# Kernel optimization log

Hardware: AMD Instinct MI355X
Metric: run time of the kernel (lower is better)

The kernel has to match this reference:

```python
import jax, jax.numpy as jnp
import numpy as np

N, D, E, K = 16384, 4096, 128, 2

def setup_inputs() -> dict:
    key = jax.random.key(0)
    k1, k2 = jax.random.split(key)
    x = jax.random.normal(k1, (N, D), dtype=jnp.float32)
    W = jax.random.normal(k2, (E, D), dtype=jnp.float32) * (1.0 / np.sqrt(D))
    b = jnp.zeros((E,), dtype=jnp.float32)
    return {"x": x, "W": W, "b": b}

def reference(x, W, b):
    # logits = x @ W.T + b  -> [N, E]
    logits = jnp.einsum('nd,ed->ne', x, W) + b
    confidence = jax.nn.sigmoid(logits)
    top_k_vals, top_k_indices = jax.lax.top_k(confidence, K)  # [N, K]
    return top_k_vals, top_k_indices
```

## Files before the change

kernel.cpp:

```cpp
#include <hip/hip_runtime.h>
#include <stdint.h>
#include <math.h>

#define N_ROWS 16384
#define D_DIM  4096
#define E_EXP  128
#define BM     32
#define BKR    128
#define NR     (D_DIM / BKR)
#define TAU    2.5e-4f

typedef short  short8 __attribute__((ext_vector_type(8)));
typedef float  f32x4  __attribute__((ext_vector_type(4)));

__device__ __forceinline__ uint32_t bf16_rne(float f) {
  uint32_t u = __builtin_bit_cast(uint32_t, f);
  return (u + 0x7fffu + ((u >> 16) & 1u)) >> 16;
}

__global__ __launch_bounds__(256) void k0_split(const float* __restrict__ W,
                                                uint16_t* __restrict__ wt) {
  const int b  = blockIdx.x;
  const int t  = threadIdx.x;
  const int eg  = b >> 5;
  const int kcg = b & 31;
  const int kc  = kcg * 4 + (t >> 6);
  const int lane = t & 63;
  const int e  = eg * 16 + (lane & 15);
  const int k0 = kc * 32 + (lane >> 4) * 8;

  const float* src = W + (size_t)e * D_DIM + k0;
  f32x4 w0 = *(const f32x4*)src;
  f32x4 w1 = *(const f32x4*)(src + 4);
  float wf[8] = {w0[0], w0[1], w0[2], w0[3], w1[0], w1[1], w1[2], w1[3]};

  uint16_t h[8], l[8];
  #pragma unroll
  for (int j = 0; j < 8; ++j) {
    uint32_t hh = bf16_rne(wf[j]);
    float hf = __builtin_bit_cast(float, hh << 16);
    h[j] = (uint16_t)hh;
    l[j] = (uint16_t)bf16_rne(wf[j] - hf);
  }
  const size_t blkh = ((size_t)(eg * 128 + kc) * 2 + 0) * 512;
  const size_t blkl = ((size_t)(eg * 128 + kc) * 2 + 1) * 512;
  *(short8*)(wt + blkh + lane * 8) = *(const short8*)h;
  *(short8*)(wt + blkl + lane * 8) = *(const short8*)l;
}

__global__ __launch_bounds__(512, 4) void k1_main(
    const float* __restrict__ x, const uint16_t* __restrict__ wt,
    const float* __restrict__ bias, float* __restrict__ out, int* __restrict__ flags)
{
  __shared__ __align__(16) uint8_t smem[32768];
  float* Ld = (float*)smem;

  const int t    = threadIdx.x;
  const int lane = t & 63;
  const int wv   = __builtin_amdgcn_readfirstlane(t >> 6);
  const int row0 = blockIdx.x * BM;

  const int srow = t >> 4;
  const int skg  = t & 15;
  const float* xp = x + (size_t)(row0 + srow) * D_DIM + skg * 8;

  const int s_w = skg >> 2, gg_w = skg & 3, rr_w = srow & 15, rg_w = srow >> 4;
  const int p_w  = gg_w * 16 + (rr_w ^ (gg_w << 1) ^ s_w);
  const int wa_h = (s_w * 4 + rg_w * 2 + 0) * 1024 + p_w * 16;
  const int wa_l = wa_h + 1024;

  const int ggr = lane >> 4, rrr = lane & 15;
  const int p_r0 = ggr * 16 + (rrr ^ (ggr << 1));

  const short8* Wt8 = (const short8*)wt;
  const int ccol = lane & 15;
  const size_t wbase0 = ((size_t)(wv * 128) * 2) * 64 + lane;

  f32x4 acc[2] = {};

  f32x4 xa0, xa1, xb0, xb1, xc0, xc1;
  xa0 = *((const f32x4*)xp + 0); xa1 = *((const f32x4*)xp + 1);
  xb0 = *((const f32x4*)(xp + BKR) + 0); xb1 = *((const f32x4*)(xp + BKR) + 1);

  short8 Wc[8], Wn[8];
  #pragma unroll
  for (int q = 0; q < 8; ++q) Wc[q] = Wt8[wbase0 + (size_t)q * 64];

  #pragma unroll 2
  for (int r = 0; r < NR; ++r) {
    if (r + 1 < NR) {
      const size_t nb = ((size_t)(wv * 128 + (r + 1) * 4) * 2) * 64 + lane;
      #pragma unroll
      for (int q = 0; q < 8; ++q) Wn[q] = Wt8[nb + (size_t)q * 64];
    }
    if (r + 2 < NR) {
      const f32x4* np = (const f32x4*)(xp + (size_t)(r + 2) * BKR);
      xc0 = np[0]; xc1 = np[1];
    }
    __builtin_amdgcn_sched_barrier(0);

    float xf[8] = {xa0[0], xa0[1], xa0[2], xa0[3], xa1[0], xa1[1], xa1[2], xa1[3]};
    uint32_t hpk[4], lpk[4];
    #pragma unroll
    for (int j = 0; j < 4; ++j) {
      uint32_t h0 = bf16_rne(xf[2*j]), h1 = bf16_rne(xf[2*j+1]);
      float h0f = __builtin_bit_cast(float, h0 << 16);
      float h1f = __builtin_bit_cast(float, h1 << 16);
      uint32_t l0 = bf16_rne(xf[2*j] - h0f), l1 = bf16_rne(xf[2*j+1] - h1f);
      hpk[j] = h0 | (h1 << 16);
      lpk[j] = l0 | (l1 << 16);
    }
    uint8_t* buf = smem + (r & 1) * 16384;
    *(uint4*)(buf + wa_h) = make_uint4(hpk[0], hpk[1], hpk[2], hpk[3]);
    *(uint4*)(buf + wa_l) = make_uint4(lpk[0], lpk[1], lpk[2], lpk[3]);

    xa0 = xb0; xa1 = xb1; xb0 = xc0; xb1 = xc1;

    asm volatile("s_waitcnt lgkmcnt(0)" ::: "memory");
    __builtin_amdgcn_s_barrier();

    __builtin_amdgcn_s_setprio(1);
    #pragma unroll
    for (int s = 0; s < 4; ++s) {
      const int pr = p_r0 ^ s;
      const short8 bh = Wc[s * 2 + 0], bl = Wc[s * 2 + 1];
      #pragma unroll
      for (int rg = 0; rg < 2; ++rg) {
        const uint8_t* fb = buf + (s * 4 + rg * 2) * 1024 + pr * 16;
        short8 ah = *(const short8*)fb;
        short8 al = *(const short8*)(fb + 1024);
        acc[rg] = __builtin_amdgcn_mfma_f32_16x16x32_bf16(ah, bh, acc[rg], 0, 0, 0);
        acc[rg] = __builtin_amdgcn_mfma_f32_16x16x32_bf16(al, bh, acc[rg], 0, 0, 0);
        acc[rg] = __builtin_amdgcn_mfma_f32_16x16x32_bf16(ah, bl, acc[rg], 0, 0, 0);
      }
    }
    __builtin_amdgcn_s_setprio(0);

    #pragma unroll
    for (int q = 0; q < 8; ++q) Wc[q] = Wn[q];
  }

  float b0 = bias[wv * 16 + ccol];
  __syncthreads();
  #pragma unroll
  for (int rg = 0; rg < 2; ++rg)
    #pragma unroll
    for (int i = 0; i < 4; ++i) {
      int row = rg * 16 + ggr * 4 + i;
      int e = wv * 16 + ccol;
      Ld[row * 128 + e] = acc[rg][i] + b0;
    }
  __syncthreads();

  {
    const int row = t >> 4, part = t & 15;
    float l1 = -3e38f, l2 = -3e38f, l3 = -3e38f;
    int   i1 = -1, i2 = -1, i3 = -1;
    auto ins = [&](float v, int e) {
      if (v > l1 || (v == l1 && e < i1)) { l3=l2; i3=i2; l2=l1; i2=i1; l1=v; i1=e; }
      else if (v > l2 || (v == l2 && e < i2)) { l3=l2; i3=i2; l2=v; i2=e; }
      else if (v > l3 || (v == l3 && e < i3)) { l3=v; i3=e; }
    };
    #pragma unroll
    for (int j = 0; j < 2; ++j) {
      const float* pp = Ld + row * 128 + part * 8 + j * 4;
      f32x4 v = *(const f32x4*)pp;
      int eb = part * 8 + j * 4;
      ins(v[0], eb); ins(v[1], eb + 1); ins(v[2], eb + 2); ins(v[3], eb + 3);
    }
    #pragma unroll
    for (int m = 1; m <= 8; m <<= 1) {
      float a1 = __shfl_xor(l1, m), a2 = __shfl_xor(l2, m), a3 = __shfl_xor(l3, m);
      int   b1i = __shfl_xor(i1, m), b2i = __shfl_xor(i2, m), b3i = __shfl_xor(i3, m);
      ins(a1, b1i); ins(a2, b2i); ins(a3, b3i);
    }
    if (part == 0) {
      int grow = row0 + row;
      int fl = ((l1 - l2) < TAU) || ((l2 - l3) < TAU);
      flags[grow] = fl;
      out[(size_t)grow * 2 + 0] = 1.f / (1.f + __expf(-l1));
      out[(size_t)grow * 2 + 1] = 1.f / (1.f + __expf(-l2));
      out[(size_t)N_ROWS * 2 + (size_t)grow * 2 + 0] = (float)i1;
      out[(size_t)N_ROWS * 2 + (size_t)grow * 2 + 1] = (float)i2;
    }
  }
}

__global__ __launch_bounds__(1024) void k2_fix(
    const float* __restrict__ x, const float* __restrict__ W,
    const float* __restrict__ bias, const int* __restrict__ flags,
    float* __restrict__ out)
{
  __shared__ double lgs[E_EXP];
  const int t    = threadIdx.x;
  const int wvi  = t >> 6, lane = t & 63;
  const int e    = wvi * 8 + (lane >> 3);
  const int sub  = lane & 7;
  const int rbase = blockIdx.x * 8;

  for (int rr = 0; rr < 8; ++rr) {
    const int row = rbase + rr;
    if (!flags[row]) continue;
    const float* xr = x + (size_t)row * D_DIM;
    const float* wr = W + (size_t)e * D_DIM;
    double a0 = 0.0, a1 = 0.0, a2 = 0.0, a3 = 0.0;
    for (int j = 0; j < 128; ++j) {
      const int c4 = (j * 8 + sub) * 4;
      f32x4 xv = *(const f32x4*)(xr + c4);
      f32x4 wvv = *(const f32x4*)(wr + c4);
      a0 += (double)xv[0] * wvv[0];
      a1 += (double)xv[1] * wvv[1];
      a2 += (double)xv[2] * wvv[2];
      a3 += (double)xv[3] * wvv[3];
    }
    double acc = (a0 + a1) + (a2 + a3);
    #pragma unroll
    for (int m = 1; m <= 4; m <<= 1) acc += __shfl_xor(acc, m);
    if (sub == 0) lgs[e] = acc + (double)bias[e];
    __syncthreads();
    if (t == 0) {
      double l1 = -1e300, l2 = -1e300; int i1 = -1, i2 = -1;
      for (int ee = 0; ee < E_EXP; ++ee) {
        double v = lgs[ee];
        if (v > l1) { l2 = l1; i2 = i1; l1 = v; i1 = ee; }
        else if (v > l2) { l2 = v; i2 = ee; }
      }
      out[(size_t)row * 2 + 0] = (float)(1.0 / (1.0 + exp(-l1)));
      out[(size_t)row * 2 + 1] = (float)(1.0 / (1.0 + exp(-l2)));
      out[(size_t)N_ROWS * 2 + (size_t)row * 2 + 0] = (float)i1;
      out[(size_t)N_ROWS * 2 + (size_t)row * 2 + 1] = (float)i2;
    }
    __syncthreads();
  }
}

extern "C" void kernel_launch(void* const* d_in, const int* in_sizes, int n_in,
                              void* d_out, int out_size, void* d_ws, size_t ws_size,
                              hipStream_t stream) {
  const float* x  = (const float*)d_in[0];
  const float* Wm = (const float*)d_in[1];
  const float* b  = (const float*)d_in[2];
  float* out = (float*)d_out;

  uint16_t* wt = (uint16_t*)d_ws;
  int* flags = (int*)((uint8_t*)d_ws + 2u * 1024 * 1024);

  k0_split<<<dim3(256), dim3(256), 0, stream>>>(Wm, wt);
  k1_main<<<dim3(N_ROWS / BM), dim3(512), 0, stream>>>(x, wt, b, out, flags);
  k2_fix<<<dim3(N_ROWS / 8), dim3(1024), 0, stream>>>(x, Wm, b, flags, out);
}
```

Measured before the change: 178.5 us.

## Stream x tiles into LDS via async global_load_lds with 4-stage ring

Replaces the register-staged prefetch of x (two tiles ahead held in VGPRs) with direct global-to-LDS async loads into a four-buffer ring, keeping three tiles in flight. Each iteration converts the raw fp32 tile from LDS into the bf16 hi/lo fragment buffer, then runs the MFMAs. The aim is deeper memory pipelining and lower VGPR pressure. In exchange, LDS per block grows from 32KB to 80KB, which limits blocks per CU, and each iteration adds an extra barrier and LDS round trip. The s_setprio hints are also removed.

```diff
diff --git a/kernel.cpp b/kernel.cpp
--- a/kernel.cpp
+++ b/kernel.cpp
@@ -12,6 +12,13 @@
 
 typedef short  short8 __attribute__((ext_vector_type(8)));
 typedef float  f32x4  __attribute__((ext_vector_type(4)));
+
+#define GAS __attribute__((address_space(1)))
+#define LAS __attribute__((address_space(3)))
+
+__device__ __forceinline__ void g2lds16(const float* g, uint8_t* l) {
+  __builtin_amdgcn_global_load_lds((const GAS uint32_t*)g, (LAS uint32_t*)l, 16, 0, 0);
+}
 
 __device__ __forceinline__ uint32_t bf16_rne(float f) {
   uint32_t u = __builtin_bit_cast(uint32_t, f);
@@ -52,19 +59,26 @@
     const float* __restrict__ x, const uint16_t* __restrict__ wt,
     const float* __restrict__ bias, float* __restrict__ out, int* __restrict__ flags)
 {
-  __shared__ __align__(16) uint8_t smem[32768];
+  __shared__ __align__(16) uint8_t smem[81920];
   float* Ld = (float*)smem;
+  uint8_t* fragb = smem + 65536;
 
   const int t    = threadIdx.x;
   const int lane = t & 63;
   const int wv   = __builtin_amdgcn_readfirstlane(t >> 6);
   const int row0 = blockIdx.x * BM;
 
-  const int srow = t >> 4;
-  const int skg  = t & 15;
-  const float* xp = x + (size_t)(row0 + srow) * D_DIM + skg * 8;
-
-  const int s_w = skg >> 2, gg_w = skg & 3, rr_w = srow & 15, rg_w = srow >> 4;
+  const int G1 = t, G2 = 512 + t;
+  const int sr1 = G1 >> 5, sg1 = (G1 & 31) ^ (sr1 & 7);
+  const int sr2 = G2 >> 5, sg2 = (G2 & 31) ^ (sr2 & 7);
+  const float* xsrc1 = x + (size_t)(row0 + sr1) * D_DIM + sg1 * 4;
+  const float* xsrc2 = x + (size_t)(row0 + sr2) * D_DIM + sg2 * 4;
+
+  const int lr = t >> 4, lg = t & 15;
+  const int rg0 = (lr * 32 + ((lg * 2 + 0) ^ (lr & 7))) * 16;
+  const int rg1 = (lr * 32 + ((lg * 2 + 1) ^ (lr & 7))) * 16;
+
+  const int s_w = lg >> 2, gg_w = lg & 3, rr_w = lr & 15, rg_w = lr >> 4;
   const int p_w  = gg_w * 16 + (rr_w ^ (gg_w << 1) ^ s_w);
   const int wa_h = (s_w * 4 + rg_w * 2 + 0) * 1024 + p_w * 16;
   const int wa_l = wa_h + 1024;
@@ -74,59 +88,71 @@
 
   const short8* Wt8 = (const short8*)wt;
   const int ccol = lane & 15;
-  const size_t wbase0 = ((size_t)(wv * 128) * 2) * 64 + lane;
 
   f32x4 acc[2] = {};
 
-  f32x4 xa0, xa1, xb0, xb1, xc0, xc1;
-  xa0 = *((const f32x4*)xp + 0); xa1 = *((const f32x4*)xp + 1);
-  xb0 = *((const f32x4*)(xp + BKR) + 0); xb1 = *((const f32x4*)(xp + BKR) + 1);
+  g2lds16(xsrc1 + 0 * BKR, smem + 0 * 16384 + G1 * 16);
+  g2lds16(xsrc2 + 0 * BKR, smem + 0 * 16384 + G2 * 16);
+  g2lds16(xsrc1 + 1 * BKR, smem + 1 * 16384 + G1 * 16);
+  g2lds16(xsrc2 + 1 * BKR, smem + 1 * 16384 + G2 * 16);
+  g2lds16(xsrc1 + 2 * BKR, smem + 2 * 16384 + G1 * 16);
+  g2lds16(xsrc2 + 2 * BKR, smem + 2 * 16384 + G2 * 16);
 
   short8 Wc[8], Wn[8];
-  #pragma unroll
-  for (int q = 0; q < 8; ++q) Wc[q] = Wt8[wbase0 + (size_t)q * 64];
+  {
+    const size_t base0 = ((size_t)(wv * 128) * 2) * 64 + lane;
+    #pragma unroll
+    for (int q = 0; q < 8; ++q) Wc[q] = Wt8[base0 + (size_t)q * 64];
+  }
 
   #pragma unroll 2
   for (int r = 0; r < NR; ++r) {
+    __builtin_amdgcn_s_barrier();
+
     if (r + 1 < NR) {
       const size_t nb = ((size_t)(wv * 128 + (r + 1) * 4) * 2) * 64 + lane;
       #pragma unroll
       for (int q = 0; q < 8; ++q) Wn[q] = Wt8[nb + (size_t)q * 64];
     }
-    if (r + 2 < NR) {
-      const f32x4* np = (const f32x4*)(xp + (size_t)(r + 2) * BKR);
-      xc0 = np[0]; xc1 = np[1];
-    }
+    if (r + 3 < NR) {
+      const int rr = r + 3;
+      uint8_t* rb = smem + (rr & 3) * 16384;
+      g2lds16(xsrc1 + (size_t)rr * BKR, rb + G1 * 16);
+      g2lds16(xsrc2 + (size_t)rr * BKR, rb + G2 * 16);
+    }
+    asm volatile("s_waitcnt vmcnt(12)" ::: "memory");
     __builtin_amdgcn_sched_barrier(0);
 
-    float xf[8] = {xa0[0], xa0[1], xa0[2], xa0[3], xa1[0], xa1[1], xa1[2], xa1[3]};
-    uint32_t hpk[4], lpk[4];
-    #pragma unroll
-    for (int j = 0; j < 4; ++j) {
-      uint32_t h0 = bf16_rne(xf[2*j]), h1 = bf16_rne(xf[2*j+1]);
-      float h0f = __builtin_bit_cast(float, h0 << 16);
-      float h1f = __builtin_bit_cast(float, h1 << 16);
-      uint32_t l0 = bf16_rne(xf[2*j] - h0f), l1 = bf16_rne(xf[2*j+1] - h1f);
-      hpk[j] = h0 | (h1 << 16);
-      lpk[j] = l0 | (l1 << 16);
-    }
-    uint8_t* buf = smem + (r & 1) * 16384;
-    *(uint4*)(buf + wa_h) = make_uint4(hpk[0], hpk[1], hpk[2], hpk[3]);
-    *(uint4*)(buf + wa_l) = make_uint4(lpk[0], lpk[1], lpk[2], lpk[3]);
-
-    xa0 = xb0; xa1 = xb1; xb0 = xc0; xb1 = xc1;
+    {
+      const uint8_t* rb = smem + (r & 3) * 16384;
+      f32x4 a = *(const f32x4*)(rb + rg0);
+      f32x4 b = *(const f32x4*)(rb + rg1);
+      float xf[8] = {a[0], a[1], a[2], a[3], b[0], b[1], b[2], b[3]};
+      uint32_t hpk[4], lpk[4];
+      #pragma unroll
+      for (int j = 0; j < 4; ++j) {
+        uint32_t h0 = bf16_rne(xf[2*j]), h1 = bf16_rne(xf[2*j+1]);
+        float h0f = __builtin_bit_cast(float, h0 << 16);
+        float h1f = __builtin_bit_cast(float, h1 << 16);
+        uint32_t l0 = bf16_rne(xf[2*j] - h0f), l1 = bf16_rne(xf[2*j+1] - h1f);
+        hpk[j] = h0 | (h1 << 16);
+        lpk[j] = l0 | (l1 << 16);
+      }
+      *(uint4*)(fragb + wa_h) = make_uint4(hpk[0], hpk[1], hpk[2], hpk[3]);
+      *(uint4*)(fragb + wa_l) = make_uint4(lpk[0], lpk[1], lpk[2], lpk[3]);
+    }
 
     asm volatile("s_waitcnt lgkmcnt(0)" ::: "memory");
     __builtin_amdgcn_s_barrier();
-
-    __builtin_amdgcn_s_setprio(1);
+    __builtin_amdgcn_sched_barrier(0);
+
     #pragma unroll
     for (int s = 0; s < 4; ++s) {
       const int pr = p_r0 ^ s;
       const short8 bh = Wc[s * 2 + 0], bl = Wc[s * 2 + 1];
       #pragma unroll
       for (int rg = 0; rg < 2; ++rg) {
-        const uint8_t* fb = buf + (s * 4 + rg * 2) * 1024 + pr * 16;
+        const uint8_t* fb = fragb + (s * 4 + rg * 2) * 1024 + pr * 16;
         short8 ah = *(const short8*)fb;
         short8 al = *(const short8*)(fb + 1024);
         acc[rg] = __builtin_amdgcn_mfma_f32_16x16x32_bf16(ah, bh, acc[rg], 0, 0, 0);
@@ -134,13 +160,13 @@
         acc[rg] = __builtin_amdgcn_mfma_f32_16x16x32_bf16(ah, bl, acc[rg], 0, 0, 0);
       }
     }
-    __builtin_amdgcn_s_setprio(0);
 
     #pragma unroll
     for (int q = 0; q < 8; ++q) Wc[q] = Wn[q];
   }
 
   float b0 = bias[wv * 16 + ccol];
+  asm volatile("s_waitcnt vmcnt(0)" ::: "memory");
   __syncthreads();
   #pragma unroll
   for (int rg = 0; rg < 2; ++rg)
```

Measured after the change: 184.5 us. 1.03x slower.

## Software-pipeline x staging so LDS writes for next tile overlap MFMA compute

Applied to the files above, without the earlier changes.

Restructures the main loop so the tile for step r+1 is converted to bf16 hi/lo and written to the other LDS buffer after the MFMAs for step r. The first tile is staged in a prologue. The x prefetch distance grows from two to three tiles ahead. The setprio/sched_barrier hints are removed. The aim is to hide the conversion, LDS-store and global-load latency behind MFMA work, at the cost of more live registers, which may reduce occupancy.

```diff
diff --git a/kernel.cpp b/kernel.cpp
--- a/kernel.cpp
+++ b/kernel.cpp
@@ -74,32 +74,12 @@
 
   const short8* Wt8 = (const short8*)wt;
   const int ccol = lane & 15;
-  const size_t wbase0 = ((size_t)(wv * 128) * 2) * 64 + lane;
 
   f32x4 acc[2] = {};
 
-  f32x4 xa0, xa1, xb0, xb1, xc0, xc1;
-  xa0 = *((const f32x4*)xp + 0); xa1 = *((const f32x4*)xp + 1);
-  xb0 = *((const f32x4*)(xp + BKR) + 0); xb1 = *((const f32x4*)(xp + BKR) + 1);
-
-  short8 Wc[8], Wn[8];
-  #pragma unroll
-  for (int q = 0; q < 8; ++q) Wc[q] = Wt8[wbase0 + (size_t)q * 64];
-
-  #pragma unroll 2
-  for (int r = 0; r < NR; ++r) {
-    if (r + 1 < NR) {
-      const size_t nb = ((size_t)(wv * 128 + (r + 1) * 4) * 2) * 64 + lane;
-      #pragma unroll
-      for (int q = 0; q < 8; ++q) Wn[q] = Wt8[nb + (size_t)q * 64];
-    }
-    if (r + 2 < NR) {
-      const f32x4* np = (const f32x4*)(xp + (size_t)(r + 2) * BKR);
-      xc0 = np[0]; xc1 = np[1];
-    }
-    __builtin_amdgcn_sched_barrier(0);
-
-    float xf[8] = {xa0[0], xa0[1], xa0[2], xa0[3], xa1[0], xa1[1], xa1[2], xa1[3]};
+  {
+    f32x4 t0 = *((const f32x4*)xp + 0), t1 = *((const f32x4*)xp + 1);
+    float xf[8] = {t0[0], t0[1], t0[2], t0[3], t1[0], t1[1], t1[2], t1[3]};
     uint32_t hpk[4], lpk[4];
     #pragma unroll
     for (int j = 0; j < 4; ++j) {
@@ -110,23 +90,55 @@
       hpk[j] = h0 | (h1 << 16);
       lpk[j] = l0 | (l1 << 16);
     }
-    uint8_t* buf = smem + (r & 1) * 16384;
-    *(uint4*)(buf + wa_h) = make_uint4(hpk[0], hpk[1], hpk[2], hpk[3]);
-    *(uint4*)(buf + wa_l) = make_uint4(lpk[0], lpk[1], lpk[2], lpk[3]);
-
-    xa0 = xb0; xa1 = xb1; xb0 = xc0; xb1 = xc1;
-
-    asm volatile("s_waitcnt lgkmcnt(0)" ::: "memory");
-    __builtin_amdgcn_s_barrier();
-
-    __builtin_amdgcn_s_setprio(1);
+    *(uint4*)(smem + wa_h) = make_uint4(hpk[0], hpk[1], hpk[2], hpk[3]);
+    *(uint4*)(smem + wa_l) = make_uint4(lpk[0], lpk[1], lpk[2], lpk[3]);
+  }
+  f32x4 xa0, xa1, xb0, xb1, xc0, xc1;
+  xa0 = *((const f32x4*)(xp + 1 * BKR) + 0); xa1 = *((const f32x4*)(xp + 1 * BKR) + 1);
+  xb0 = *((const f32x4*)(xp + 2 * BKR) + 0); xb1 = *((const f32x4*)(xp + 2 * BKR) + 1);
+  xc0 = *((const f32x4*)(xp + 3 * BKR) + 0); xc1 = *((const f32x4*)(xp + 3 * BKR) + 1);
+
+  short8 Wc[8], Wn[8];
+  {
+    const size_t b0 = ((size_t)(wv * 128) * 2) * 64 + lane;
+    #pragma unroll
+    for (int q = 0; q < 8; ++q) Wc[q] = Wt8[b0 + (size_t)q * 64];
+  }
+  asm volatile("s_waitcnt lgkmcnt(0)" ::: "memory");
+  __builtin_amdgcn_s_barrier();
+
+  #pragma unroll 2
+  for (int r = 0; r < NR; ++r) {
+    uint8_t* rbuf = smem + (r & 1) * 16384;
+    uint8_t* wbuf = smem + ((r + 1) & 1) * 16384;
+
+    if (r + 1 < NR) {
+      const size_t nb = ((size_t)(wv * 128 + (r + 1) * 4) * 2) * 64 + lane;
+      #pragma unroll
+      for (int q = 0; q < 8; ++q) Wn[q] = Wt8[nb + (size_t)q * 64];
+    }
+
+    uint32_t hpk[4], lpk[4];
+    if (r + 1 < NR) {
+      float xf[8] = {xa0[0], xa0[1], xa0[2], xa0[3], xa1[0], xa1[1], xa1[2], xa1[3]};
+      #pragma unroll
+      for (int j = 0; j < 4; ++j) {
+        uint32_t h0 = bf16_rne(xf[2*j]), h1 = bf16_rne(xf[2*j+1]);
+        float h0f = __builtin_bit_cast(float, h0 << 16);
+        float h1f = __builtin_bit_cast(float, h1 << 16);
+        uint32_t l0 = bf16_rne(xf[2*j] - h0f), l1 = bf16_rne(xf[2*j+1] - h1f);
+        hpk[j] = h0 | (h1 << 16);
+        lpk[j] = l0 | (l1 << 16);
+      }
+    }
+
     #pragma unroll
     for (int s = 0; s < 4; ++s) {
       const int pr = p_r0 ^ s;
       const short8 bh = Wc[s * 2 + 0], bl = Wc[s * 2 + 1];
       #pragma unroll
       for (int rg = 0; rg < 2; ++rg) {
-        const uint8_t* fb = buf + (s * 4 + rg * 2) * 1024 + pr * 16;
+        const uint8_t* fb = rbuf + (s * 4 + rg * 2) * 1024 + pr * 16;
         short8 ah = *(const short8*)fb;
         short8 al = *(const short8*)(fb + 1024);
         acc[rg] = __builtin_amdgcn_mfma_f32_16x16x32_bf16(ah, bh, acc[rg], 0, 0, 0);
@@ -134,7 +146,20 @@
         acc[rg] = __builtin_amdgcn_mfma_f32_16x16x32_bf16(ah, bl, acc[rg], 0, 0, 0);
       }
     }
-    __builtin_amdgcn_s_setprio(0);
+
+    if (r + 1 < NR) {
+      *(uint4*)(wbuf + wa_h) = make_uint4(hpk[0], hpk[1], hpk[2], hpk[3]);
+      *(uint4*)(wbuf + wa_l) = make_uint4(lpk[0], lpk[1], lpk[2], lpk[3]);
+    }
+
+    xa0 = xb0; xa1 = xb1; xb0 = xc0; xb1 = xc1;
+    if (r + 4 < NR) {
+      const f32x4* np = (const f32x4*)(xp + (size_t)(r + 4) * BKR);
+      xc0 = np[0]; xc1 = np[1];
+    }
+
+    asm volatile("s_waitcnt lgkmcnt(0)" ::: "memory");
+    __builtin_amdgcn_s_barrier();
 
     #pragma unroll
     for (int q = 0; q < 8; ++q) Wc[q] = Wn[q];
```

Result: faster. 170.8 us (-4.3%).

## Stage x tiles via async global-to-LDS loads with triple buffer and LDS counter sync

Applied to the files above, without the earlier changes.

The main kernel now handles 64 rows per block. Each wave computes a 32-row by 32-expert quadrant, so every W fragment it loads feeds two row groups. Raw fp32 x tiles are copied straight into a swizzled three-slot LDS ring with global_load_lds. Each wave does its own bf16 hi/lo split after reading from LDS, and W fragments are loaded per step instead of being double-buffered in registers. Block-wide barriers are replaced by spin-waits on LDS atomic counters (staged/done), aiming for better load/compute overlap. The trade-offs are more LDS per block (about 96KB) and therefore lower occupancy, redundant hi/lo conversion work, and spin-wait overhead.

```diff
diff --git a/kernel.cpp b/kernel.cpp
--- a/kernel.cpp
+++ b/kernel.cpp
@@ -5,13 +5,21 @@
 #define N_ROWS 16384
 #define D_DIM  4096
 #define E_EXP  128
-#define BM     32
+#define BM     64
 #define BKR    128
 #define NR     (D_DIM / BKR)
+#define NW     8
 #define TAU    2.5e-4f
 
 typedef short  short8 __attribute__((ext_vector_type(8)));
 typedef float  f32x4  __attribute__((ext_vector_type(4)));
+
+#define GAS __attribute__((address_space(1)))
+#define LAS __attribute__((address_space(3)))
+
+__device__ __forceinline__ void g2lds16(const float* g, uint8_t* l) {
+  __builtin_amdgcn_global_load_lds((const GAS uint32_t*)g, (LAS uint32_t*)l, 16, 0, 0);
+}
 
 __device__ __forceinline__ uint32_t bf16_rne(float f) {
   uint32_t u = __builtin_bit_cast(uint32_t, f);
@@ -48,112 +56,131 @@
   *(short8*)(wt + blkl + lane * 8) = *(const short8*)l;
 }
 
-__global__ __launch_bounds__(512, 4) void k1_main(
+__global__ __launch_bounds__(512) void k1_main(
     const float* __restrict__ x, const uint16_t* __restrict__ wt,
     const float* __restrict__ bias, float* __restrict__ out, int* __restrict__ flags)
 {
-  __shared__ __align__(16) uint8_t smem[32768];
+  __shared__ __align__(16) uint8_t smem[3 * 32768 + 256];
+  int* done   = (int*)(smem + 98304);
+  int* staged = done + 32;
   float* Ld = (float*)smem;
 
   const int t    = threadIdx.x;
   const int lane = t & 63;
   const int wv   = __builtin_amdgcn_readfirstlane(t >> 6);
+  const int rh   = wv >> 2;
+  const int eq   = wv & 3;
   const int row0 = blockIdx.x * BM;
-
-  const int srow = t >> 4;
-  const int skg  = t & 15;
-  const float* xp = x + (size_t)(row0 + srow) * D_DIM + skg * 8;
-
-  const int s_w = skg >> 2, gg_w = skg & 3, rr_w = srow & 15, rg_w = srow >> 4;
-  const int p_w  = gg_w * 16 + (rr_w ^ (gg_w << 1) ^ s_w);
-  const int wa_h = (s_w * 4 + rg_w * 2 + 0) * 1024 + p_w * 16;
-  const int wa_l = wa_h + 1024;
-
-  const int ggr = lane >> 4, rrr = lane & 15;
-  const int p_r0 = ggr * 16 + (rrr ^ (ggr << 1));
+  const int r15  = lane & 15, kg = lane >> 4;
 
   const short8* Wt8 = (const short8*)wt;
-  const int ccol = lane & 15;
-  const size_t wbase0 = ((size_t)(wv * 128) * 2) * 64 + lane;
-
-  f32x4 acc[2] = {};
-
-  f32x4 xa0, xa1, xb0, xb1, xc0, xc1;
-  xa0 = *((const f32x4*)xp + 0); xa1 = *((const f32x4*)xp + 1);
-  xb0 = *((const f32x4*)(xp + BKR) + 0); xb1 = *((const f32x4*)(xp + BKR) + 1);
-
-  short8 Wc[8], Wn[8];
-  #pragma unroll
-  for (int q = 0; q < 8; ++q) Wc[q] = Wt8[wbase0 + (size_t)q * 64];
-
-  #pragma unroll 2
+
+  auto stageTile = [&](int tile) {
+    uint8_t* base = smem + (tile % 3) * 32768;
+    #pragma unroll
+    for (int i = 0; i < 4; ++i) {
+      const int G  = wv * 256 + i * 64 + lane;
+      const int rr = G >> 5, gp = G & 31;
+      const int gs = gp ^ (rr & 7);
+      const float* src = x + (size_t)(row0 + rr) * D_DIM + (size_t)tile * BKR + gs * 4;
+      g2lds16(src, base + (size_t)G * 16);
+    }
+  };
+
+  if (t < 64) ((int*)(smem + 98304))[t] = 0;
+  __syncthreads();
+  stageTile(0);
+  stageTile(1);
+  asm volatile("s_waitcnt vmcnt(0)" ::: "memory");
+  if (lane == 0) { atomicAdd(&staged[0], 1); atomicAdd(&staged[1], 1); }
+
+  f32x4 acc[2][2] = {};
+
   for (int r = 0; r < NR; ++r) {
-    if (r + 1 < NR) {
-      const size_t nb = ((size_t)(wv * 128 + (r + 1) * 4) * 2) * 64 + lane;
+    {
+      volatile int* vs = (volatile int*)staged;
+      while (vs[r] < NW) __builtin_amdgcn_s_sleep(2);
+      asm volatile("" ::: "memory");
+      __builtin_amdgcn_sched_barrier(0);
+    }
+
+    if (r + 2 < NR) {
+      if (r >= 1) {
+        volatile int* vd = (volatile int*)done;
+        while (vd[r - 1] < NW) __builtin_amdgcn_s_sleep(2);
+        asm volatile("" ::: "memory");
+        __builtin_amdgcn_sched_barrier(0);
+      }
+      stageTile(r + 2);
+    }
+
+    const uint8_t* slot = smem + (r % 3) * 32768;
+    #pragma unroll
+    for (int s = 0; s < 4; ++s) {
+      const int kcg = r * 4 + s;
+      short8 bh[2], bl[2];
       #pragma unroll
-      for (int q = 0; q < 8; ++q) Wn[q] = Wt8[nb + (size_t)q * 64];
-    }
-    if (r + 2 < NR) {
-      const f32x4* np = (const f32x4*)(xp + (size_t)(r + 2) * BKR);
-      xc0 = np[0]; xc1 = np[1];
-    }
-    __builtin_amdgcn_sched_barrier(0);
-
-    float xf[8] = {xa0[0], xa0[1], xa0[2], xa0[3], xa1[0], xa1[1], xa1[2], xa1[3]};
-    uint32_t hpk[4], lpk[4];
-    #pragma unroll
-    for (int j = 0; j < 4; ++j) {
-      uint32_t h0 = bf16_rne(xf[2*j]), h1 = bf16_rne(xf[2*j+1]);
-      float h0f = __builtin_bit_cast(float, h0 << 16);
-      float h1f = __builtin_bit_cast(float, h1 << 16);
-      uint32_t l0 = bf16_rne(xf[2*j] - h0f), l1 = bf16_rne(xf[2*j+1] - h1f);
-      hpk[j] = h0 | (h1 << 16);
-      lpk[j] = l0 | (l1 << 16);
-    }
-    uint8_t* buf = smem + (r & 1) * 16384;
-    *(uint4*)(buf + wa_h) = make_uint4(hpk[0], hpk[1], hpk[2], hpk[3]);
-    *(uint4*)(buf + wa_l) = make_uint4(lpk[0], lpk[1], lpk[2], lpk[3]);
-
-    xa0 = xb0; xa1 = xb1; xb0 = xc0; xb1 = xc1;
-
-    asm volatile("s_waitcnt lgkmcnt(0)" ::: "memory");
-    __builtin_amdgcn_s_barrier();
-
-    __builtin_amdgcn_s_setprio(1);
-    #pragma unroll
-    for (int s = 0; s < 4; ++s) {
-      const int pr = p_r0 ^ s;
-      const short8 bh = Wc[s * 2 + 0], bl = Wc[s * 2 + 1];
+      for (int egi = 0; egi < 2; ++egi) {
+        const size_t bb = ((size_t)((eq * 2 + egi) * 128 + kcg) * 2) * 64 + lane;
+        bh[egi] = Wt8[bb];
+        bl[egi] = Wt8[bb + 64];
+      }
       #pragma unroll
       for (int rg = 0; rg < 2; ++rg) {
-        const uint8_t* fb = buf + (s * 4 + rg * 2) * 1024 + pr * 16;
-        short8 ah = *(const short8*)fb;
-        short8 al = *(const short8*)(fb + 1024);
-        acc[rg] = __builtin_amdgcn_mfma_f32_16x16x32_bf16(ah, bh, acc[rg], 0, 0, 0);
-        acc[rg] = __builtin_amdgcn_mfma_f32_16x16x32_bf16(al, bh, acc[rg], 0, 0, 0);
-        acc[rg] = __builtin_amdgcn_mfma_f32_16x16x32_bf16(ah, bl, acc[rg], 0, 0, 0);
-      }
-    }
-    __builtin_amdgcn_s_setprio(0);
-
-    #pragma unroll
-    for (int q = 0; q < 8; ++q) Wc[q] = Wn[q];
-  }
-
-  float b0 = bias[wv * 16 + ccol];
+        const int rr = rh * 32 + rg * 16 + r15;
+        const int m  = rr & 7;
+        const int g0 = s * 8 + kg * 2;
+        f32x4 A = *(const f32x4*)(slot + ((size_t)rr * 32 + (g0 ^ m)) * 16);
+        f32x4 B = *(const f32x4*)(slot + ((size_t)rr * 32 + ((g0 + 1) ^ m)) * 16);
+        float xf[8] = {A[0], A[1], A[2], A[3], B[0], B[1], B[2], B[3]};
+        uint32_t hpk[4], lpk[4];
+        #pragma unroll
+        for (int j = 0; j < 4; ++j) {
+          uint32_t h0 = bf16_rne(xf[2*j]), h1 = bf16_rne(xf[2*j+1]);
+          float h0f = __builtin_bit_cast(float, h0 << 16);
+          float h1f = __builtin_bit_cast(float, h1 << 16);
+          uint32_t l0 = bf16_rne(xf[2*j] - h0f), l1 = bf16_rne(xf[2*j+1] - h1f);
+          hpk[j] = h0 | (h1 << 16);
+          lpk[j] = l0 | (l1 << 16);
+        }
+        short8 ah = __builtin_bit_cast(short8, make_uint4(hpk[0], hpk[1], hpk[2], hpk[3]));
+        short8 al = __builtin_bit_cast(short8, make_uint4(lpk[0], lpk[1], lpk[2], lpk[3]));
+        #pragma unroll
+        for (int egi = 0; egi < 2; ++egi) {
+          acc[rg][egi] = __builtin_amdgcn_mfma_f32_16x16x32_bf16(ah, bh[egi], acc[rg][egi], 0, 0, 0);
+          acc[rg][egi] = __builtin_amdgcn_mfma_f32_16x16x32_bf16(al, bh[egi], acc[rg][egi], 0, 0, 0);
+          acc[rg][egi] = __builtin_amdgcn_mfma_f32_16x16x32_bf16(ah, bl[egi], acc[rg][egi], 0, 0, 0);
+        }
+      }
+    }
+
+    asm volatile("s_waitcnt lgkmcnt(0)" ::: "memory");
+    asm volatile("s_waitcnt vmcnt(0)" ::: "memory");
+    if (lane == 0) {
+      atomicAdd(&done[r], 1);
+      if (r + 2 < NR) atomicAdd(&staged[r + 2], 1);
+    }
+  }
+
   __syncthreads();
-  #pragma unroll
-  for (int rg = 0; rg < 2; ++rg)
-    #pragma unroll
-    for (int i = 0; i < 4; ++i) {
-      int row = rg * 16 + ggr * 4 + i;
-      int e = wv * 16 + ccol;
-      Ld[row * 128 + e] = acc[rg][i] + b0;
-    }
+  {
+    float b0 = bias[eq * 32 + r15];
+    float b1 = bias[eq * 32 + 16 + r15];
+    #pragma unroll
+    for (int rg = 0; rg < 2; ++rg)
+      #pragma unroll
+      for (int egi = 0; egi < 2; ++egi)
+        #pragma unroll
+        for (int i = 0; i < 4; ++i) {
+          int rl = rh * 32 + rg * 16 + kg * 4 + i;
+          int e  = (eq * 2 + egi) * 16 + r15;
+          Ld[rl * 128 + e] = acc[rg][egi][i] + (egi ? b1 : b0);
+        }
+  }
   __syncthreads();
 
   {
-    const int row = t >> 4, part = t & 15;
+    const int row = t >> 3, part = t & 7;
     float l1 = -3e38f, l2 = -3e38f, l3 = -3e38f;
     int   i1 = -1, i2 = -1, i3 = -1;
     auto ins = [&](float v, int e) {
@@ -162,14 +189,15 @@
       else if (v > l3 || (v == l3 && e < i3)) { l3=v; i3=e; }
     };
     #pragma unroll
-    for (int j = 0; j < 2; ++j) {
-      const float* pp = Ld + row * 128 + part * 8 + j * 4;
+    for (int jj = 0; jj < 4; ++jj) {
+      int j = (jj + t) & 3;
+      const float* pp = Ld + row * 128 + part * 16 + j * 4;
       f32x4 v = *(const f32x4*)pp;
-      int eb = part * 8 + j * 4;
+      int eb = part * 16 + j * 4;
       ins(v[0], eb); ins(v[1], eb + 1); ins(v[2], eb + 2); ins(v[3], eb + 3);
     }
     #pragma unroll
-    for (int m = 1; m <= 8; m <<= 1) {
+    for (int m = 1; m <= 4; m <<= 1) {
       float a1 = __shfl_xor(l1, m), a2 = __shfl_xor(l2, m), a3 = __shfl_xor(l3, m);
       int   b1i = __shfl_xor(i1, m), b2i = __shfl_xor(i2, m), b3i = __shfl_xor(i3, m);
       ins(a1, b1i); ins(a2, b2i); ins(a3, b3i);
```

Result: slower. 213.6 us (+19.7%).
